# Optimization experiments

Measured on AMD Instinct MI355X. Metric: run time of the kernel, lower is better.

The kernel has to match this reference:

```python
import jax, jax.numpy as jnp
import numpy as np

N = 100000
E = 3200000
NFEAT = 256
NHID = 128
NCLASS = 16
TEXT_CNT = 50000


def setup_inputs() -> dict:
    key = jax.random.key(0)
    ks = jax.random.split(key, 12)
    x = jax.random.normal(ks[0], (N, NFEAT), dtype=jnp.float32)
    adj_rows = jax.random.randint(ks[1], (E,), 0, N, dtype=jnp.int32)
    adj_cols = jax.random.randint(ks[2], (E,), 0, N, dtype=jnp.int32)
    # positive normalized-adjacency-like weights (~1/avg_degree scale)
    adj_vals = jax.random.uniform(ks[3], (E,), dtype=jnp.float32) / 32.0
    W1 = jax.random.normal(ks[4], (NFEAT, NHID), dtype=jnp.float32) / np.sqrt(NFEAT)
    b1 = jax.random.normal(ks[5], (NHID,), dtype=jnp.float32) * 0.01
    W2 = jax.random.normal(ks[6], (NHID, NFEAT), dtype=jnp.float32) / np.sqrt(NHID)
    b2 = jax.random.normal(ks[7], (NFEAT,), dtype=jnp.float32) * 0.01
    cW1 = jax.random.normal(ks[8], (NFEAT, NCLASS), dtype=jnp.float32) / np.sqrt(NFEAT)
    cb1 = jax.random.normal(ks[9], (NCLASS,), dtype=jnp.float32) * 0.01
    cW2 = jax.random.normal(ks[10], (NFEAT, NCLASS), dtype=jnp.float32) / np.sqrt(NFEAT)
    cb2 = jax.random.normal(ks[11], (NCLASS,), dtype=jnp.float32) * 0.01
    return {"x": x, "adj_rows": adj_rows, "adj_cols": adj_cols, "adj_vals": adj_vals,
            "W1": W1, "b1": b1, "W2": W2, "b2": b2,
            "cW1": cW1, "cb1": cb1, "cW2": cw2 if (cw2 := None) else cW2, "cb2": cb2}


def spmm(rows, cols, vals, dense):
    # out[r] = sum_{e: rows[e]==r} vals[e] * dense[cols[e]]   (COO SpMM)
    gathered = vals[:, None] * dense[cols]  # [E, D]
    return jax.ops.segment_sum(gathered, rows, num_segments=N)


def reference(x, adj_rows, adj_cols, adj_vals, W1, b1, W2, b2, cW1, cb1, cW2, cb2):
    # gc1: adj @ (x @ W1) + b1, then ReLU (dropout is identity at inference)
    h = jax.nn.relu(spmm(adj_rows, adj_cols, adj_vals, x @ W1) + b1)  # [N, NHID]
    # gc2: adj @ (h @ W2) + b2
    out = spmm(adj_rows, adj_cols, adj_vals, h @ W2) + b2  # [N, NFEAT]
    text_cls = out[:TEXT_CNT] @ cW1 + cb1  # [TEXT_CNT, NCLASS]
    img_cls = out[TEXT_CNT:] @ cW2 + cb2   # [N-TEXT_CNT, NCLASS]
    return (out, text_cls, img_cls)
```

## Files before the change

### kernel.cpp

```cpp
#include <hip/hip_runtime.h>

#define N_NODES  100000
#define N_EDGES  3200000
#define NFEAT    256
#define NHID     128
#define NCLASS   16
#define TEXT_CNT 50000

#define RPB      256
#define NB       ((N_NODES + RPB - 1) / RPB)
#define CAP      16384
#define SC_EDGES 8192
#define SC_BLKS  ((N_EDGES + SC_EDGES - 1) / SC_EDGES)
#define FN_CAPL  9216
#define COLHALF  (N_NODES / 2)

typedef unsigned int uint;
typedef __bf16 bf16x8 __attribute__((ext_vector_type(8)));
typedef __bf16 bf16x4 __attribute__((ext_vector_type(4)));
typedef float f32x4 __attribute__((ext_vector_type(4)));

__device__ inline uint bf16_rne(float f) {
  uint u = __float_as_uint(f);
  return (u + 0x7fffu + ((u >> 16) & 1u)) >> 16;
}
__device__ inline float bf_lo(uint u) { return __uint_as_float(u << 16); }
__device__ inline float bf_hi(uint u) { return __uint_as_float(u & 0xffff0000u); }


__global__ __launch_bounds__(256) void prep_kernel(const float* __restrict__ W1,
                                                   const float* __restrict__ W2,
                                                   const float* __restrict__ b2,
                                                   const float* __restrict__ cW1,
                                                   const float* __restrict__ cb1,
                                                   const float* __restrict__ cW2,
                                                   const float* __restrict__ cb2,
                                                   unsigned short* __restrict__ W1t,
                                                   unsigned short* __restrict__ W2t,
                                                   float* __restrict__ Wc1, float* __restrict__ bc1,
                                                   float* __restrict__ Wc2, float* __restrict__ bc2,
                                                   int* __restrict__ gcursor) {
  int idx = blockIdx.x * 256 + threadIdx.x;
  if (idx < 32768) {
    int n = idx >> 8, k = idx & 255;
    W1t[idx] = (unsigned short)bf16_rne(W1[(size_t)k * NHID + n]);
  } else if (idx < 65536) {
    int i2 = idx - 32768;
    int n = i2 >> 7, k = i2 & 127;
    W2t[i2] = (unsigned short)bf16_rne(W2[(size_t)k * NFEAT + n]);
  } else if (idx < 69632) {
    int e = idx - 65536;
    int set = e >> 11;
    int e2 = e & 2047;
    int i = e2 >> 4, c = e2 & 15;
    const float* cw = set ? cW2 : cW1;
    float acc = 0.f;
    for (int k = 0; k < NFEAT; ++k)
      acc += W2[(size_t)i * NFEAT + k] * cw[k * NCLASS + c];
    (set ? Wc2 : Wc1)[e2] = acc;
    if (e < 32) {
      int s2 = e >> 4, c2 = e & 15;
      const float* cwb = s2 ? cW2 : cW1;
      float b = (s2 ? cb2 : cb1)[c2];
      for (int k = 0; k < NFEAT; ++k) b += b2[k] * cwb[k * NCLASS + c2];
      (s2 ? bc2 : bc1)[c2] = b;
    }
  } else if (idx < 69632 + NB) {
    int b = idx - 69632;
    gcursor[b] = b * CAP;
  }
}


__global__ __launch_bounds__(512) void scatter_sort_kernel(const int* __restrict__ rows,
                                                           const int* __restrict__ cols,
                                                           const float* __restrict__ vals,
                                                           int* __restrict__ gcursor,
                                                           int2* __restrict__ packedA, int E) {
  __shared__ int2 eds[SC_EDGES];
  __shared__ int hist[512];
  __shared__ int bcnt[NB];
  __shared__ int lofs[NB];
  __shared__ int lcur[NB];
  __shared__ int gofs[NB];
  int t = threadIdx.x;
  int base = blockIdx.x * SC_EDGES;
  hist[t] = 0;
  __syncthreads();
#pragma unroll
  for (int i = 0; i < SC_EDGES / 512; ++i) {
    int e = base + i * 512 + t;
    if (e < E) atomicAdd(&hist[rows[e] >> 8], 1);
  }
  __syncthreads();
  int v = hist[t];
  if (t < NB) bcnt[t] = v;
  __syncthreads();
  for (int off = 1; off < 512; off <<= 1) {
    int u = (t >= off) ? hist[t - off] : 0;
    __syncthreads();
    hist[t] += u;
    __syncthreads();
  }
  if (t < NB) {
    int ex = hist[t] - v;
    lofs[t] = ex;
    lcur[t] = ex;
    gofs[t] = v ? atomicAdd(&gcursor[t], v) : 0;
  }
  __syncthreads();
#pragma unroll
  for (int i = 0; i < SC_EDGES / 512; ++i) {
    int e = base + i * 512 + t;
    if (e < E) {
      int r = rows[e];
      int b = r >> 8;
      int p = atomicAdd(&lcur[b], 1);
      eds[p] = make_int2(((r & 255) << 17) | cols[e], __float_as_int(vals[e]));
    }
  }
  __syncthreads();
  int wid = t >> 6, lane = t & 63;
  for (int b = wid; b < NB; b += 8) {
    int cnt = bcnt[b];
    int lo = lofs[b];
    int go = gofs[b];
    int lim = (b + 1) << 14;
    for (int j = lane; j < cnt; j += 64)
      if (go + j < lim) packedA[go + j] = eds[lo + j];
  }
}


__global__ __launch_bounds__(512) void csr_finalize_kernel(const int* __restrict__ gcursor,
                                                           const int2* __restrict__ packedA,
                                                           int2* __restrict__ packedB,
                                                           int* __restrict__ row_ptr) {
  __shared__ int2 eds[FN_CAPL];
  __shared__ int pre[512];
  __shared__ int kh[512];
  __shared__ int kofs[512];
  __shared__ int kcur[512];
  int b = blockIdx.x;
  int t = threadIdx.x;
  int cntt = (t < NB) ? (gcursor[t] - t * CAP) : 0;
  pre[t] = cntt;
  __syncthreads();
  for (int off = 1; off < 512; off <<= 1) {
    int u = (t >= off) ? pre[t - off] : 0;
    __syncthreads();
    pre[t] += u;
    __syncthreads();
  }
  int cnt = gcursor[b] - b * CAP;
  int gout = pre[b] - cnt;
  int s0 = b * CAP;
  int end = s0 + cnt;
  kh[t] = 0;
  __syncthreads();
  for (int i = s0 + t; i < end; i += 512) {
    int2 pk = packedA[i];
    int key = ((pk.x >> 17) << 1) | ((pk.x & 0x1FFFF) >= COLHALF);
    atomicAdd(&kh[key], 1);
  }
  __syncthreads();
  int v = kh[t];
  kofs[t] = v;
  __syncthreads();
  for (int off = 1; off < 512; off <<= 1) {
    int u = (t >= off) ? kofs[t - off] : 0;
    __syncthreads();
    kofs[t] += u;
    __syncthreads();
  }
  kcur[t] = kofs[t] - v;
  __syncthreads();
  if (t < RPB) {
    int row = b * RPB + t;
    if (row < N_NODES) row_ptr[row] = gout + kcur[2 * t];
  }
  if (b == 0 && t == 0) row_ptr[N_NODES] = N_EDGES;
  __syncthreads();
  if (cnt <= FN_CAPL) {
    for (int i = s0 + t; i < end; i += 512) {
      int2 pk = packedA[i];
      int key = ((pk.x >> 17) << 1) | ((pk.x & 0x1FFFF) >= COLHALF);
      int p = atomicAdd(&kcur[key], 1);
      eds[p] = pk;
    }
    __syncthreads();
    for (int i = t; i < cnt; i += 512) {
      int2 pk = eds[i];
      packedB[gout + i] = make_int2((pk.x & 0x1FFFF) << 8, pk.y);
    }
  } else {
    for (int i = s0 + t; i < end; i += 512) {
      int2 pk = packedA[i];
      int key = ((pk.x >> 17) << 1) | ((pk.x & 0x1FFFF) >= COLHALF);
      int p = atomicAdd(&kcur[key], 1);
      packedB[gout + p] = make_int2((pk.x & 0x1FFFF) << 8, pk.y);
    }
  }
}


template <int A_FP32, int OUT_BF16, int K, int N, int MT>
__device__ __forceinline__ void gemm_body(int bx, int by, const void* __restrict__ Aptr,
                                          const __bf16* __restrict__ Bt,
                                          const float* __restrict__ bias,
                                          void* __restrict__ Cptr, int M,
                                          __bf16* __restrict__ As, __bf16* __restrict__ Bs) {
  constexpr int BM = MT * 32;
  int tid = threadIdx.x;
  int lane = tid & 63;
  int w = tid >> 6;
  int wr = w >> 1, wc = w & 1;
  int brow = bx * BM;
  int bcol = by * 128;
  int r16 = lane & 15, kb = lane >> 4;

  f32x4 acc[MT][4];
#pragma unroll
  for (int m = 0; m < MT; ++m)
#pragma unroll
    for (int n = 0; n < 4; ++n) acc[m][n] = (f32x4){0.f, 0.f, 0.f, 0.f};

  float4 pa[MT];
  bf16x8 pah[MT / 2];
  bf16x8 pb[2];

  auto loadA = [&](int k0) {
    if (A_FP32) {
      const float* A = (const float*)Aptr;
#pragma unroll
      for (int i = 0; i < MT; ++i) {
        int idx = tid + i * 256;
        int row = idx >> 3;
        int kq = (idx & 7) << 2;
        int gr = brow + row;
        pa[i] = make_float4(0.f, 0.f, 0.f, 0.f);
        if (gr < M) pa[i] = *(const float4*)&A[(size_t)gr * K + k0 + kq];
      }
    } else {
      const __bf16* A = (const __bf16*)Aptr;
#pragma unroll
      for (int i = 0; i < MT / 2; ++i) {
        int idx = tid + i * 256;
        int row = idx >> 2;
        int kq = (idx & 3) << 3;
        int gr = brow + row;
        bf16x8 vv = {};
        if (gr < M) vv = *(const bf16x8*)&A[(size_t)gr * K + k0 + kq];
        pah[i] = vv;
      }
    }
  };
  auto loadB = [&](int k0) {
#pragma unroll
    for (int i = 0; i < 2; ++i) {
      int idx = tid + i * 256;
      int col = idx >> 2;
      int kq = (idx & 3) << 3;
      pb[i] = *(const bf16x8*)&Bt[(size_t)(bcol + col) * K + k0 + kq];
    }
  };
  auto storeAB = [&]() {
    if (A_FP32) {
#pragma unroll
      for (int i = 0; i < MT; ++i) {
        int idx = tid + i * 256;
        int row = idx >> 3;
        int kq = (idx & 7) << 2;
        bf16x4 o;
        o[0] = (__bf16)pa[i].x; o[1] = (__bf16)pa[i].y;
        o[2] = (__bf16)pa[i].z; o[3] = (__bf16)pa[i].w;
        *(bf16x4*)&As[row * 40 + kq] = o;
      }
    } else {
#pragma unroll
      for (int i = 0; i < MT / 2; ++i) {
        int idx = tid + i * 256;
        int row = idx >> 2;
        int kq = (idx & 3) << 3;
        *(bf16x8*)&As[row * 40 + kq] = pah[i];
      }
    }
#pragma unroll
    for (int i = 0; i < 2; ++i) {
      int idx = tid + i * 256;
      int col = idx >> 2;
      int kq = (idx & 3) << 3;
      *(bf16x8*)&Bs[col * 40 + kq] = pb[i];
    }
  };

  loadA(0);
  loadB(0);
  for (int k0 = 0; k0 < K; k0 += 32) {
    storeAB();
    __syncthreads();
    if (k0 + 32 < K) { loadA(k0 + 32); loadB(k0 + 32); }
    bf16x8 a[MT], b[4];
#pragma unroll
    for (int m = 0; m < MT; ++m)
      a[m] = *(bf16x8*)&As[(wr * (BM / 2) + m * 16 + r16) * 40 + kb * 8];
#pragma unroll
    for (int n = 0; n < 4; ++n)
      b[n] = *(bf16x8*)&Bs[(wc * 64 + n * 16 + r16) * 40 + kb * 8];
#pragma unroll
    for (int m = 0; m < MT; ++m)
#pragma unroll
      for (int n = 0; n < 4; ++n)
        acc[m][n] = __builtin_amdgcn_mfma_f32_16x16x32_bf16(a[m], b[n], acc[m][n], 0, 0, 0);
    __syncthreads();
  }

  int crow0 = brow + wr * (BM / 2);
  int ccol0 = bcol + wc * 64;
#pragma unroll
  for (int n = 0; n < 4; ++n) {
    int col = ccol0 + n * 16 + r16;
    float bv = bias ? bias[col] : 0.f;
#pragma unroll
    for (int m = 0; m < MT; ++m) {
#pragma unroll
      for (int r = 0; r < 4; ++r) {
        int row = crow0 + m * 16 + kb * 4 + r;
        if (row < M) {
          float val = acc[m][n][r] + bv;
          if (OUT_BF16)
            ((unsigned short*)Cptr)[(size_t)row * N + col] = (unsigned short)bf16_rne(val);
          else
            ((float*)Cptr)[(size_t)row * N + col] = val;
        }
      }
    }
  }
}


template <int A_FP32, int OUT_BF16, int K, int N, int MT>
__global__ __launch_bounds__(256) void gemm_mfma_kernel(const void* __restrict__ Aptr,
                                                        const __bf16* __restrict__ Bt,
                                                        const float* __restrict__ bias,
                                                        void* __restrict__ Cptr, int M) {
  __shared__ __align__(16) __bf16 smem[2 * 128 * 40];
  gemm_body<A_FP32, OUT_BF16, K, N, MT>(blockIdx.x, blockIdx.y, Aptr, Bt, bias, Cptr, M,
                                        smem, smem + 128 * 40);
}


#define FMA4(Gv0, Gv1, Gv2, Gv3, Vv0, Vv1, Vv2, Vv3)                                   \
  a0 += Vv0 * bf_lo(Gv0.x); a1 += Vv0 * bf_hi(Gv0.x);                                  \
  a2 += Vv0 * bf_lo(Gv0.y); a3 += Vv0 * bf_hi(Gv0.y);                                  \
  a0 += Vv1 * bf_lo(Gv1.x); a1 += Vv1 * bf_hi(Gv1.x);                                  \
  a2 += Vv1 * bf_lo(Gv1.y); a3 += Vv1 * bf_hi(Gv1.y);                                  \
  a0 += Vv2 * bf_lo(Gv2.x); a1 += Vv2 * bf_hi(Gv2.x);                                  \
  a2 += Vv2 * bf_lo(Gv2.y); a3 += Vv2 * bf_hi(Gv2.y);                                  \
  a0 += Vv3 * bf_lo(Gv3.x); a1 += Vv3 * bf_hi(Gv3.x);                                  \
  a2 += Vv3 * bf_lo(Gv3.y); a3 += Vv3 * bf_hi(Gv3.y);

__global__ __launch_bounds__(256) void spmm_bf16_kernel(const int* __restrict__ row_ptr,
                                                        const int2* __restrict__ packed,
                                                        const uint* __restrict__ src,
                                                        uint* __restrict__ dst,
                                                        const float* __restrict__ bias,
                                                        int relu, int nrows) {
  int tid = threadIdx.x;
  int lane = tid & 63;
  int half = lane >> 5;
  int l32 = lane & 31;
  int row = blockIdx.x * 4 + (tid >> 6);
  if (row >= nrows) return;
  int s = row_ptr[row];
  int e = row_ptr[row + 1];
  const char* srcb = (const char*)src + (l32 << 3);
  float a0 = 0.f, a1 = 0.f, a2 = 0.f, a3 = 0.f;
  int i = s;

  if (e - s >= 16) {
    int2 A0 = packed[i + 0 + half], A1 = packed[i + 2 + half];
    int2 A2 = packed[i + 4 + half], A3 = packed[i + 6 + half];
    uint2 G0 = *(const uint2*)(srcb + (uint)A0.x);
    uint2 G1 = *(const uint2*)(srcb + (uint)A1.x);
    uint2 G2 = *(const uint2*)(srcb + (uint)A2.x);
    uint2 G3 = *(const uint2*)(srcb + (uint)A3.x);
    float W0 = __int_as_float(A0.y), W1 = __int_as_float(A1.y);
    float W2 = __int_as_float(A2.y), W3 = __int_as_float(A3.y);
    int2 B0 = packed[i + 8 + half], B1 = packed[i + 10 + half];
    int2 B2 = packed[i + 12 + half], B3 = packed[i + 14 + half];
    i += 16;
    for (; i + 8 <= e; i += 8) {
      uint2 H0 = *(const uint2*)(srcb + (uint)B0.x);
      uint2 H1 = *(const uint2*)(srcb + (uint)B1.x);
      uint2 H2 = *(const uint2*)(srcb + (uint)B2.x);
      uint2 H3 = *(const uint2*)(srcb + (uint)B3.x);
      float X0 = __int_as_float(B0.y), X1 = __int_as_float(B1.y);
      float X2 = __int_as_float(B2.y), X3 = __int_as_float(B3.y);
      B0 = packed[i + 0 + half]; B1 = packed[i + 2 + half];
      B2 = packed[i + 4 + half]; B3 = packed[i + 6 + half];
      FMA4(G0, G1, G2, G3, W0, W1, W2, W3)
      G0 = H0; G1 = H1; G2 = H2; G3 = H3;
      W0 = X0; W1 = X1; W2 = X2; W3 = X3;
    }
    FMA4(G0, G1, G2, G3, W0, W1, W2, W3)
    {
      uint2 H0 = *(const uint2*)(srcb + (uint)B0.x);
      uint2 H1 = *(const uint2*)(srcb + (uint)B1.x);
      uint2 H2 = *(const uint2*)(srcb + (uint)B2.x);
      uint2 H3 = *(const uint2*)(srcb + (uint)B3.x);
      float X0 = __int_as_float(B0.y), X1 = __int_as_float(B1.y);
      float X2 = __int_as_float(B2.y), X3 = __int_as_float(B3.y);
      FMA4(H0, H1, H2, H3, X0, X1, X2, X3)
    }
  }
  for (; i + 8 <= e; i += 8) {
    int2 m0 = packed[i + 0 + half], m1 = packed[i + 2 + half];
    int2 m2 = packed[i + 4 + half], m3 = packed[i + 6 + half];
    uint2 u0 = *(const uint2*)(srcb + (uint)m0.x);
    uint2 u1 = *(const uint2*)(srcb + (uint)m1.x);
    uint2 u2 = *(const uint2*)(srcb + (uint)m2.x);
    uint2 u3 = *(const uint2*)(srcb + (uint)m3.x);
    float v0 = __int_as_float(m0.y), v1 = __int_as_float(m1.y);
    float v2 = __int_as_float(m2.y), v3 = __int_as_float(m3.y);
    FMA4(u0, u1, u2, u3, v0, v1, v2, v3)
  }
  for (; i + 4 <= e; i += 4) {
    int2 m0 = packed[i + 0 + half], m1 = packed[i + 2 + half];
    uint2 u0 = *(const uint2*)(srcb + (uint)m0.x);
    uint2 u1 = *(const uint2*)(srcb + (uint)m1.x);
    float v0 = __int_as_float(m0.y), v1 = __int_as_float(m1.y);
    a0 += v0 * bf_lo(u0.x); a1 += v0 * bf_hi(u0.x); a2 += v0 * bf_lo(u0.y); a3 += v0 * bf_hi(u0.y);
    a0 += v1 * bf_lo(u1.x); a1 += v1 * bf_hi(u1.x); a2 += v1 * bf_lo(u1.y); a3 += v1 * bf_hi(u1.y);
  }
  for (; i < e; i += 2) {
    int ee = i + half;
    int ok = ee < e;
    int2 m = packed[ok ? ee : (e - 1)];
    uint2 u = *(const uint2*)(srcb + (uint)m.x);
    float v = ok ? __int_as_float(m.y) : 0.f;
    a0 += v * bf_lo(u.x); a1 += v * bf_hi(u.x); a2 += v * bf_lo(u.y); a3 += v * bf_hi(u.y);
  }
  a0 += __shfl_xor(a0, 32); a1 += __shfl_xor(a1, 32);
  a2 += __shfl_xor(a2, 32); a3 += __shfl_xor(a3, 32);
  if (half == 0) {
    if (bias) {
      a0 += bias[4 * l32 + 0]; a1 += bias[4 * l32 + 1];
      a2 += bias[4 * l32 + 2]; a3 += bias[4 * l32 + 3];
    }
    if (relu) {
      a0 = fmaxf(a0, 0.f); a1 = fmaxf(a1, 0.f);
      a2 = fmaxf(a2, 0.f); a3 = fmaxf(a3, 0.f);
    }
    uint2 o;
    o.x = bf16_rne(a0) | (bf16_rne(a1) << 16);
    o.y = bf16_rne(a2) | (bf16_rne(a3) << 16);
    *(uint2*)&dst[(size_t)row * 64 + l32 * 2] = o;
  }
}


__device__ __forceinline__ void cls_body(int bid, int clsblks,
                                         const uint* __restrict__ t3,
                                         const float* __restrict__ Wc1,
                                         const float* __restrict__ bc1,
                                         const float* __restrict__ Wc2,
                                         const float* __restrict__ bc2,
                                         float* __restrict__ out1,
                                         float* __restrict__ out2) {
  int half = clsblks >> 1;
  int region = bid >= half;
  int b = region ? bid - half : bid;
  const float* Wc = region ? Wc2 : Wc1;
  const float* bc = region ? bc2 : bc1;
  float* outp = region ? out2 : out1;
  int row0 = region ? TEXT_CNT : 0;
  int nrows = region ? (N_NODES - TEXT_CNT) : TEXT_CNT;

  int lane = threadIdx.x & 63;
  int wav = b * 4 + (threadIdx.x >> 6);
  int nw = half * 4;
  int c = lane & 15;
  int kg = lane >> 4;
  float w[32];
#pragma unroll
  for (int j = 0; j < 32; ++j) w[j] = Wc[(kg * 32 + j) * NCLASS + c];
  float bcv = bc[c];
  for (int r = wav; r < nrows; r += nw) {
    const uint4* rp = (const uint4*)&t3[(size_t)(row0 + r) * 64 + kg * 16];
    float acc = 0.f;
#pragma unroll
    for (int qq = 0; qq < 4; ++qq) {
      uint4 u = rp[qq];
      acc += bf_lo(u.x) * w[qq * 8 + 0] + bf_hi(u.x) * w[qq * 8 + 1]
           + bf_lo(u.y) * w[qq * 8 + 2] + bf_hi(u.y) * w[qq * 8 + 3]
           + bf_lo(u.z) * w[qq * 8 + 4] + bf_hi(u.z) * w[qq * 8 + 5]
           + bf_lo(u.w) * w[qq * 8 + 6] + bf_hi(u.w) * w[qq * 8 + 7];
    }
    acc += __shfl_xor(acc, 16);
    acc += __shfl_xor(acc, 32);
    if (lane < 16) outp[(size_t)r * NCLASS + lane] = acc + bcv;
  }
}


__global__ __launch_bounds__(256) void fused_g2c_kernel(const uint* __restrict__ t3u,
                                                        const __bf16* __restrict__ W2t,
                                                        const float* __restrict__ b2,
                                                        float* __restrict__ outp,
                                                        const float* __restrict__ Wc1,
                                                        const float* __restrict__ bc1,
                                                        const float* __restrict__ Wc2,
                                                        const float* __restrict__ bc2,
                                                        float* __restrict__ out1,
                                                        float* __restrict__ out2,
                                                        int g2blks, int clsblks) {
  __shared__ __align__(16) __bf16 smem[2 * 128 * 40];
  if ((int)blockIdx.x < g2blks) {
    int bx = blockIdx.x >> 1;
    int by = blockIdx.x & 1;
    gemm_body<0, 0, NHID, NFEAT, 4>(bx, by, t3u, W2t, b2, outp, N_NODES,
                                    smem, smem + 128 * 40);
  } else {
    cls_body(blockIdx.x - g2blks, clsblks, t3u, Wc1, bc1, Wc2, bc2, out1, out2);
  }
}


extern "C" void kernel_launch(void* const* d_in, const int* in_sizes, int n_in,
                              void* d_out, int out_size, void* d_ws, size_t ws_size,
                              hipStream_t stream) {
  const float* x     = (const float*)d_in[0];
  const int*   arows = (const int*)d_in[1];
  const int*   acols = (const int*)d_in[2];
  const float* avals = (const float*)d_in[3];
  const float* W1    = (const float*)d_in[4];
  const float* b1    = (const float*)d_in[5];
  const float* W2    = (const float*)d_in[6];
  const float* b2    = (const float*)d_in[7];
  const float* cW1   = (const float*)d_in[8];
  const float* cb1   = (const float*)d_in[9];
  const float* cW2   = (const float*)d_in[10];
  const float* cb2   = (const float*)d_in[11];
  float* outp = (float*)d_out;

  char* ws = (char*)d_ws;
  size_t off = 0;
  auto alloc = [&](size_t bytes) -> void* {
    void* p = ws + off;
    off += (bytes + 255) & ~(size_t)255;
    return p;
  };
  uint*  t1u     = (uint*) alloc((size_t)N_NODES * 64 * 4);
  uint*  hu      = (uint*) alloc((size_t)N_NODES * 64 * 4);
  uint*  t3u     = (uint*) alloc((size_t)N_NODES * 64 * 4);
  int2*  packedA = (int2*) alloc((size_t)NB * CAP * 8);
  int2*  packedB = (int2*) alloc((size_t)N_EDGES * 8);
  int*   gcursor = (int*)  alloc((size_t)NB * 4);
  int*   rowp    = (int*)  alloc((size_t)(N_NODES + 1) * 4);
  unsigned short* W1t = (unsigned short*)alloc((size_t)NHID * NFEAT * 2);
  unsigned short* W2t = (unsigned short*)alloc((size_t)NFEAT * NHID * 2);
  float* Wc1     = (float*)alloc(NHID * NCLASS * 4);
  float* Wc2     = (float*)alloc(NHID * NCLASS * 4);
  float* bc1     = (float*)alloc(64);
  float* bc2     = (float*)alloc(64);

  prep_kernel<<<(69632 + NB + 255) / 256, 256, 0, stream>>>(
      W1, W2, b2, cW1, cb1, cW2, cb2, W1t, W2t, Wc1, bc1, Wc2, bc2, gcursor);

  scatter_sort_kernel<<<SC_BLKS, 512, 0, stream>>>(arows, acols, avals, gcursor, packedA, N_EDGES);

  csr_finalize_kernel<<<NB, 512, 0, stream>>>(gcursor, packedA, packedB, rowp);

  int mblk64 = (N_NODES + 63) / 64;
  gemm_mfma_kernel<1, 1, NFEAT, NHID, 2><<<dim3(mblk64, 1), 256, 0, stream>>>(
      x, (const __bf16*)W1t, nullptr, t1u, N_NODES);

  int sblk = (N_NODES + 3) / 4;
  spmm_bf16_kernel<<<sblk, 256, 0, stream>>>(rowp, packedB, t1u, hu, b1, 1, N_NODES);
  spmm_bf16_kernel<<<sblk, 256, 0, stream>>>(rowp, packedB, hu, t3u, nullptr, 0, N_NODES);

  int mblk = (N_NODES + 127) / 128;
  int g2blks = mblk * 2;
  int clsblks = 2048;
  fused_g2c_kernel<<<g2blks + clsblks, 256, 0, stream>>>(
      t3u, (const __bf16*)W2t, b2, outp, Wc1, bc1, Wc2, bc2,
      outp + (size_t)N_NODES * NFEAT,
      outp + (size_t)N_NODES * NFEAT + (size_t)TEXT_CNT * NCLASS,
      g2blks, clsblks);
}
```

Baseline: 404.4 us.

## Fuse edge scatter-sort with first GEMM in one launch and shrink tiles

The edge scatter-sort and the x@W1 MFMA GEMM now run in a single 512-thread launch, sharing dynamic LDS. Scatter blocks and paired GEMM tiles execute side by side, so the memory-bound sort and the compute-bound GEMM can overlap and one launch is removed. The edges handled per scatter block are halved so that block fits the shared LDS budget and more blocks are spawned. The second GEMM moves from 128-row to 64-row tiles, giving more blocks with less work each. The cost is more atomic and global traffic from the smaller scatter chunks, and possible LDS-driven occupancy limits in the fused kernel.

Result: faster. 394.4 us (-2.5%).

```diff
diff --git a/kernel.cpp b/kernel.cpp
--- a/kernel.cpp
+++ b/kernel.cpp
@@ -10,10 +10,11 @@
 #define RPB      256
 #define NB       ((N_NODES + RPB - 1) / RPB)
 #define CAP      16384
-#define SC_EDGES 8192
+#define SC_EDGES 4096
 #define SC_BLKS  ((N_EDGES + SC_EDGES - 1) / SC_EDGES)
 #define FN_CAPL  9216
 #define COLHALF  (N_NODES / 2)
+#define FUS_LDS  41072
 
 typedef unsigned int uint;
 typedef __bf16 bf16x8 __attribute__((ext_vector_type(8)));
@@ -72,19 +73,20 @@
 }
 
 
-__global__ __launch_bounds__(512) void scatter_sort_kernel(const int* __restrict__ rows,
-                                                           const int* __restrict__ cols,
-                                                           const float* __restrict__ vals,
-                                                           int* __restrict__ gcursor,
-                                                           int2* __restrict__ packedA, int E) {
-  __shared__ int2 eds[SC_EDGES];
-  __shared__ int hist[512];
-  __shared__ int bcnt[NB];
-  __shared__ int lofs[NB];
-  __shared__ int lcur[NB];
-  __shared__ int gofs[NB];
+__device__ __forceinline__ void scatter_body(int bx, const int* __restrict__ rows,
+                                             const int* __restrict__ cols,
+                                             const float* __restrict__ vals,
+                                             int* __restrict__ gcursor,
+                                             int2* __restrict__ packedA, int E,
+                                             char* __restrict__ dynbuf) {
+  int2* eds = (int2*)dynbuf;
+  int* hist = (int*)(dynbuf + 32768);
+  int* bcnt = hist + 512;
+  int* lofs = bcnt + NB;
+  int* lcur = lofs + NB;
+  int* gofs = lcur + NB;
   int t = threadIdx.x;
-  int base = blockIdx.x * SC_EDGES;
+  int base = bx * SC_EDGES;
   hist[t] = 0;
   __syncthreads();
 #pragma unroll
@@ -128,6 +130,161 @@
     int lim = (b + 1) << 14;
     for (int j = lane; j < cnt; j += 64)
       if (go + j < lim) packedA[go + j] = eds[lo + j];
+  }
+}
+
+
+template <int A_FP32, int OUT_BF16, int K, int N, int MT>
+__device__ __forceinline__ void gemm_body(int bx, int by, const void* __restrict__ Aptr,
+                                          const __bf16* __restrict__ Bt,
+                                          const float* __restrict__ bias,
+                                          void* __restrict__ Cptr, int M, int tid,
+                                          __bf16* __restrict__ As, __bf16* __restrict__ Bs) {
+  constexpr int BM = MT * 32;
+  int lane = tid & 63;
+  int w = tid >> 6;
+  int wr = w >> 1, wc = w & 1;
+  int brow = bx * BM;
+  int bcol = by * 128;
+  int r16 = lane & 15, kb = lane >> 4;
+
+  f32x4 acc[MT][4];
+#pragma unroll
+  for (int m = 0; m < MT; ++m)
+#pragma unroll
+    for (int n = 0; n < 4; ++n) acc[m][n] = (f32x4){0.f, 0.f, 0.f, 0.f};
+
+  float4 pa[MT];
+  bf16x8 pah[MT / 2];
+  bf16x8 pb[2];
+
+  auto loadA = [&](int k0) {
+    if (A_FP32) {
+      const float* A = (const float*)Aptr;
+#pragma unroll
+      for (int i = 0; i < MT; ++i) {
+        int idx = tid + i * 256;
+        int row = idx >> 3;
+        int kq = (idx & 7) << 2;
+        int gr = brow + row;
+        pa[i] = make_float4(0.f, 0.f, 0.f, 0.f);
+        if (gr < M) pa[i] = *(const float4*)&((const float*)Aptr)[(size_t)gr * K + k0 + kq];
+        (void)A;
+      }
+    } else {
+      const __bf16* A = (const __bf16*)Aptr;
+#pragma unroll
+      for (int i = 0; i < MT / 2; ++i) {
+        int idx = tid + i * 256;
+        int row = idx >> 2;
+        int kq = (idx & 3) << 3;
+        int gr = brow + row;
+        bf16x8 vv = {};
+        if (gr < M) vv = *(const bf16x8*)&A[(size_t)gr * K + k0 + kq];
+        pah[i] = vv;
+      }
+    }
+  };
+  auto loadB = [&](int k0) {
+#pragma unroll
+    for (int i = 0; i < 2; ++i) {
+      int idx = tid + i * 256;
+      int col = idx >> 2;
+      int kq = (idx & 3) << 3;
+      pb[i] = *(const bf16x8*)&Bt[(size_t)(bcol + col) * K + k0 + kq];
+    }
+  };
+  auto storeAB = [&]() {
+    if (A_FP32) {
+#pragma unroll
+      for (int i = 0; i < MT; ++i) {
+        int idx = tid + i * 256;
+        int row = idx >> 3;
+        int kq = (idx & 7) << 2;
+        bf16x4 o;
+        o[0] = (__bf16)pa[i].x; o[1] = (__bf16)pa[i].y;
+        o[2] = (__bf16)pa[i].z; o[3] = (__bf16)pa[i].w;
+        *(bf16x4*)&As[row * 40 + kq] = o;
+      }
+    } else {
+#pragma unroll
+      for (int i = 0; i < MT / 2; ++i) {
+        int idx = tid + i * 256;
+        int row = idx >> 2;
+        int kq = (idx & 3) << 3;
+        *(bf16x8*)&As[row * 40 + kq] = pah[i];
+      }
+    }
+#pragma unroll
+    for (int i = 0; i < 2; ++i) {
+      int idx = tid + i * 256;
+      int col = idx >> 2;
+      int kq = (idx & 3) << 3;
+      *(bf16x8*)&Bs[col * 40 + kq] = pb[i];
+    }
+  };
+
+  loadA(0);
+  loadB(0);
+  for (int k0 = 0; k0 < K; k0 += 32) {
+    storeAB();
+    __syncthreads();
+    if (k0 + 32 < K) { loadA(k0 + 32); loadB(k0 + 32); }
+    bf16x8 a[MT], b[4];
+#pragma unroll
+    for (int m = 0; m < MT; ++m)
+      a[m] = *(bf16x8*)&As[(wr * (BM / 2) + m * 16 + r16) * 40 + kb * 8];
+#pragma unroll
+    for (int n = 0; n < 4; ++n)
+      b[n] = *(bf16x8*)&Bs[(wc * 64 + n * 16 + r16) * 40 + kb * 8];
+#pragma unroll
+    for (int m = 0; m < MT; ++m)
+#pragma unroll
+      for (int n = 0; n < 4; ++n)
+        acc[m][n] = __builtin_amdgcn_mfma_f32_16x16x32_bf16(a[m], b[n], acc[m][n], 0, 0, 0);
+    __syncthreads();
+  }
+
+  int crow0 = brow + wr * (BM / 2);
+  int ccol0 = bcol + wc * 64;
+#pragma unroll
+  for (int n = 0; n < 4; ++n) {
+    int col = ccol0 + n * 16 + r16;
+    float bv = bias ? bias[col] : 0.f;
+#pragma unroll
+    for (int m = 0; m < MT; ++m) {
+#pragma unroll
+      for (int r = 0; r < 4; ++r) {
+        int row = crow0 + m * 16 + kb * 4 + r;
+        if (row < M) {
+          float val = acc[m][n][r] + bv;
+          if (OUT_BF16)
+            ((unsigned short*)Cptr)[(size_t)row * N + col] = (unsigned short)bf16_rne(val);
+          else
+            ((float*)Cptr)[(size_t)row * N + col] = val;
+        }
+      }
+    }
+  }
+}
+
+
+__global__ __launch_bounds__(512) void fused_sg1_kernel(
+    const int* __restrict__ rows, const int* __restrict__ cols, const float* __restrict__ vals,
+    int* __restrict__ gcursor, int2* __restrict__ packedA, int E,
+    const float* __restrict__ x, const __bf16* __restrict__ W1t, uint* __restrict__ t1u,
+    int M, int mblk64) {
+  extern __shared__ __align__(16) char dynbuf[];
+  if ((int)blockIdx.x < SC_BLKS) {
+    scatter_body(blockIdx.x, rows, cols, vals, gcursor, packedA, E, dynbuf);
+  } else {
+    int p = blockIdx.x - SC_BLKS;
+    int sub = threadIdx.x >> 8;
+    int tile = p * 2 + sub;
+    int tidl = threadIdx.x & 255;
+    __bf16* As = (__bf16*)(dynbuf + sub * 15360);
+    __bf16* Bs = As + 64 * 40;
+    gemm_body<1, 1, NFEAT, NHID, 2>(tile, 0, x, W1t, nullptr, t1u, M, tidl, As, Bs);
   }
 }
 
@@ -201,152 +358,6 @@
       packedB[gout + p] = make_int2((pk.x & 0x1FFFF) << 8, pk.y);
     }
   }
-}
-
-
-template <int A_FP32, int OUT_BF16, int K, int N, int MT>
-__device__ __forceinline__ void gemm_body(int bx, int by, const void* __restrict__ Aptr,
-                                          const __bf16* __restrict__ Bt,
-                                          const float* __restrict__ bias,
-                                          void* __restrict__ Cptr, int M,
-                                          __bf16* __restrict__ As, __bf16* __restrict__ Bs) {
-  constexpr int BM = MT * 32;
-  int tid = threadIdx.x;
-  int lane = tid & 63;
-  int w = tid >> 6;
-  int wr = w >> 1, wc = w & 1;
-  int brow = bx * BM;
-  int bcol = by * 128;
-  int r16 = lane & 15, kb = lane >> 4;
-
-  f32x4 acc[MT][4];
-#pragma unroll
-  for (int m = 0; m < MT; ++m)
-#pragma unroll
-    for (int n = 0; n < 4; ++n) acc[m][n] = (f32x4){0.f, 0.f, 0.f, 0.f};
-
-  float4 pa[MT];
-  bf16x8 pah[MT / 2];
-  bf16x8 pb[2];
-
-  auto loadA = [&](int k0) {
-    if (A_FP32) {
-      const float* A = (const float*)Aptr;
-#pragma unroll
-      for (int i = 0; i < MT; ++i) {
-        int idx = tid + i * 256;
-        int row = idx >> 3;
-        int kq = (idx & 7) << 2;
-        int gr = brow + row;
-        pa[i] = make_float4(0.f, 0.f, 0.f, 0.f);
-        if (gr < M) pa[i] = *(const float4*)&A[(size_t)gr * K + k0 + kq];
-      }
-    } else {
-      const __bf16* A = (const __bf16*)Aptr;
-#pragma unroll
-      for (int i = 0; i < MT / 2; ++i) {
-        int idx = tid + i * 256;
-        int row = idx >> 2;
-        int kq = (idx & 3) << 3;
-        int gr = brow + row;
-        bf16x8 vv = {};
-        if (gr < M) vv = *(const bf16x8*)&A[(size_t)gr * K + k0 + kq];
-        pah[i] = vv;
-      }
-    }
-  };
-  auto loadB = [&](int k0) {
-#pragma unroll
-    for (int i = 0; i < 2; ++i) {
-      int idx = tid + i * 256;
-      int col = idx >> 2;
-      int kq = (idx & 3) << 3;
-      pb[i] = *(const bf16x8*)&Bt[(size_t)(bcol + col) * K + k0 + kq];
-    }
-  };
-  auto storeAB = [&]() {
-    if (A_FP32) {
-#pragma unroll
-      for (int i = 0; i < MT; ++i) {
-        int idx = tid + i * 256;
-        int row = idx >> 3;
-        int kq = (idx & 7) << 2;
-        bf16x4 o;
-        o[0] = (__bf16)pa[i].x; o[1] = (__bf16)pa[i].y;
-        o[2] = (__bf16)pa[i].z; o[3] = (__bf16)pa[i].w;
-        *(bf16x4*)&As[row * 40 + kq] = o;
-      }
-    } else {
-#pragma unroll
-      for (int i = 0; i < MT / 2; ++i) {
-        int idx = tid + i * 256;
-        int row = idx >> 2;
-        int kq = (idx & 3) << 3;
-        *(bf16x8*)&As[row * 40 + kq] = pah[i];
-      }
-    }
-#pragma unroll
-    for (int i = 0; i < 2; ++i) {
-      int idx = tid + i * 256;
-      int col = idx >> 2;
-      int kq = (idx & 3) << 3;
-      *(bf16x8*)&Bs[col * 40 + kq] = pb[i];
-    }
-  };
-
-  loadA(0);
-  loadB(0);
-  for (int k0 = 0; k0 < K; k0 += 32) {
-    storeAB();
-    __syncthreads();
-    if (k0 + 32 < K) { loadA(k0 + 32); loadB(k0 + 32); }
-    bf16x8 a[MT], b[4];
-#pragma unroll
-    for (int m = 0; m < MT; ++m)
-      a[m] = *(bf16x8*)&As[(wr * (BM / 2) + m * 16 + r16) * 40 + kb * 8];
-#pragma unroll
-    for (int n = 0; n < 4; ++n)
-      b[n] = *(bf16x8*)&Bs[(wc * 64 + n * 16 + r16) * 40 + kb * 8];
-#pragma unroll
-    for (int m = 0; m < MT; ++m)
-#pragma unroll
-      for (int n = 0; n < 4; ++n)
-        acc[m][n] = __builtin_amdgcn_mfma_f32_16x16x32_bf16(a[m], b[n], acc[m][n], 0, 0, 0);
-    __syncthreads();
-  }
-
-  int crow0 = brow + wr * (BM / 2);
-  int ccol0 = bcol + wc * 64;
-#pragma unroll
-  for (int n = 0; n < 4; ++n) {
-    int col = ccol0 + n * 16 + r16;
-    float bv = bias ? bias[col] : 0.f;
-#pragma unroll
-    for (int m = 0; m < MT; ++m) {
-#pragma unroll
-      for (int r = 0; r < 4; ++r) {
-        int row = crow0 + m * 16 + kb * 4 + r;
-        if (row < M) {
-          float val = acc[m][n][r] + bv;
-          if (OUT_BF16)
-            ((unsigned short*)Cptr)[(size_t)row * N + col] = (unsigned short)bf16_rne(val);
-          else
-            ((float*)Cptr)[(size_t)row * N + col] = val;
-        }
-      }
-    }
-  }
-}
-
-
-template <int A_FP32, int OUT_BF16, int K, int N, int MT>
-__global__ __launch_bounds__(256) void gemm_mfma_kernel(const void* __restrict__ Aptr,
-                                                        const __bf16* __restrict__ Bt,
-                                                        const float* __restrict__ bias,
-                                                        void* __restrict__ Cptr, int M) {
-  __shared__ __align__(16) __bf16 smem[2 * 128 * 40];
-  gemm_body<A_FP32, OUT_BF16, K, N, MT>(blockIdx.x, blockIdx.y, Aptr, Bt, bias, Cptr, M,
-                                        smem, smem + 128 * 40);
 }
 
 
@@ -515,12 +526,12 @@
                                                         float* __restrict__ out1,
                                                         float* __restrict__ out2,
                                                         int g2blks, int clsblks) {
-  __shared__ __align__(16) __bf16 smem[2 * 128 * 40];
+  __shared__ __align__(16) __bf16 smem[64 * 40 + 128 * 40];
   if ((int)blockIdx.x < g2blks) {
     int bx = blockIdx.x >> 1;
     int by = blockIdx.x & 1;
-    gemm_body<0, 0, NHID, NFEAT, 4>(bx, by, t3u, W2t, b2, outp, N_NODES,
-                                    smem, smem + 128 * 40);
+    gemm_body<0, 0, NHID, NFEAT, 2>(bx, by, t3u, W2t, b2, outp, N_NODES, threadIdx.x,
+                                    smem, smem + 64 * 40);
   } else {
     cls_body(blockIdx.x - g2blks, clsblks, t3u, Wc1, bc1, Wc2, bc2, out1, out2);
   }
@@ -568,20 +579,19 @@
   prep_kernel<<<(69632 + NB + 255) / 256, 256, 0, stream>>>(
       W1, W2, b2, cW1, cb1, cW2, cb2, W1t, W2t, Wc1, bc1, Wc2, bc2, gcursor);
 
-  scatter_sort_kernel<<<SC_BLKS, 512, 0, stream>>>(arows, acols, avals, gcursor, packedA, N_EDGES);
+  int mblk64 = (N_NODES + 63) / 64;
+  int gpairs = (mblk64 + 1) / 2;
+  fused_sg1_kernel<<<SC_BLKS + gpairs, 512, FUS_LDS, stream>>>(
+      arows, acols, avals, gcursor, packedA, N_EDGES,
+      x, (const __bf16*)W1t, t1u, N_NODES, mblk64);
 
   csr_finalize_kernel<<<NB, 512, 0, stream>>>(gcursor, packedA, packedB, rowp);
-
-  int mblk64 = (N_NODES + 63) / 64;
-  gemm_mfma_kernel<1, 1, NFEAT, NHID, 2><<<dim3(mblk64, 1), 256, 0, stream>>>(
-      x, (const __bf16*)W1t, nullptr, t1u, N_NODES);
 
   int sblk = (N_NODES + 3) / 4;
   spmm_bf16_kernel<<<sblk, 256, 0, stream>>>(rowp, packedB, t1u, hu, b1, 1, N_NODES);
   spmm_bf16_kernel<<<sblk, 256, 0, stream>>>(rowp, packedB, hu, t3u, nullptr, 0, N_NODES);
 
-  int mblk = (N_NODES + 127) / 128;
-  int g2blks = mblk * 2;
+  int g2blks = mblk64 * 2;
   int clsblks = 2048;
   fused_g2c_kernel<<<g2blks + clsblks, 256, 0, stream>>>(
       t3u, (const __bf16*)W2t, b2, outp, Wc1, bc1, Wc2, bc2,
```
